# Optimization experiments

Hardware: AMD Instinct MI355X
Metric: run time of the kernel (lower is better)

Reference implementation:

```python
import jax, jax.numpy as jnp
import numpy as np

H = 256  # hidden size

def setup_inputs() -> dict:
    key = jax.random.key(0)
    k1, k2, k3 = jax.random.split(key, 3)
    B, T, D = 64, 2048, 256
    x = jax.random.normal(k1, (B, T, D), dtype=jnp.float32)
    Wx = jax.random.normal(k2, (D, 4 * H), dtype=jnp.float32) * (1.0 / np.sqrt(D))
    Wh = jax.random.normal(k3, (H, 4 * H), dtype=jnp.float32) * (1.0 / np.sqrt(H))
    bx = jnp.zeros((4 * H,), dtype=jnp.float32)
    bh = jnp.zeros((4 * H,), dtype=jnp.float32)
    return {"x": x, "Wx": Wx, "Wh": Wh, "bx": bx, "bh": bh}

def reference(x, Wx, Wh, bx, bh):
    B, T, D = x.shape
    # Precompute input projections for all timesteps: [T, B, 4H]
    xg = jnp.einsum('btd,dg->tbg', x, Wx) + bx

    def step(carry, xg_t):
        h_prev, c_prev = carry
        gates = xg_t + h_prev @ Wh + bh          # [B, 4H]
        f, i, o, chat = jnp.split(gates, 4, axis=-1)
        f_t = jax.nn.sigmoid(f)
        i_t = jax.nn.sigmoid(i)
        o_t = jax.nn.sigmoid(o)
        c_t = f_t * c_prev + i_t * jnp.tanh(chat)
        h_t = o_t * jnp.tanh(c_t)
        return (h_t, c_t), h_t

    h0 = jnp.zeros((B, H), dtype=x.dtype)
    c0 = jnp.zeros((B, H), dtype=x.dtype)
    (h_T, c_T), hs = jax.lax.scan(step, (h0, c0), xg)  # hs: [T, B, H]
    outputs = jnp.transpose(hs, (1, 0, 2))  # batch_first: [B, T, H]
    return outputs, (h_T, c_T)
```

## Files before the change

kernel.cpp:

```cpp
#include <hip/hip_runtime.h>
#include <stdint.h>

#define H 256
#define BB 64
#define TT 2048
#define G4 1024
#define LDX 264

typedef __attribute__((ext_vector_type(8))) short short8;
typedef __attribute__((ext_vector_type(4))) float float4_;
typedef unsigned long long ull;
typedef unsigned short ushort_t;
typedef unsigned int uint_t;

static __device__ __forceinline__ float bfhi2f(ushort_t u) {
    union { unsigned int i; float f; } v; v.i = ((unsigned int)u) << 16; return v.f;
}
static __device__ __forceinline__ ushort_t f2bf(float x) {
    union { float f; unsigned int i; } v; v.f = x;
    unsigned int u = v.i;
    return (ushort_t)((u + 0x7FFFu + ((u >> 16) & 1u)) >> 16);
}
static __device__ __forceinline__ void split2(float x, ushort_t& hi, ushort_t& lo) {
    hi = f2bf(x);
    lo = f2bf(x - bfhi2f(hi));
}
static __device__ __forceinline__ float sigm(float x) { return 1.0f / (1.0f + __expf(-x)); }
static __device__ __forceinline__ float tanh_(float x) { return 2.0f / (1.0f + __expf(-2.0f * x)) - 1.0f; }

__global__ __launch_bounds__(256) void split_w(const float* __restrict__ Wx,
                                               const float* __restrict__ Wh,
                                               ushort_t* __restrict__ planes) {
    const int g = blockIdx.x & 1023;
    const int mat = blockIdx.x >> 10;
    const int k = threadIdx.x;
    const float* src = mat ? Wh : Wx;
    float v = src[(size_t)k * G4 + g];
    ushort_t hi, lo; split2(v, hi, lo);
    ushort_t* ph = planes + (size_t)mat * 2 * G4 * 256;
    ph[g * 256 + k] = hi;
    ph[(size_t)G4 * 256 + g * 256 + k] = lo;
}

__global__ __launch_bounds__(256, 1) void lstm_scan(
        const float* __restrict__ x,
        const float* __restrict__ bx,
        const float* __restrict__ bh,
        const ushort_t* __restrict__ WxTh, const ushort_t* __restrict__ WxTl,
        const ushort_t* __restrict__ WhTh, const ushort_t* __restrict__ WhTl,
        float* __restrict__ out0,
        float* __restrict__ outh,
        float* __restrict__ outc,
        uint_t* __restrict__ hbuf,
        uint_t* __restrict__ ctrl) {
    __shared__ ushort_t xah[16 * LDX], xal[16 * LDX];
    __shared__ ushort_t hsh[16 * LDX], hsl[16 * LDX];
    __shared__ float gatesL[1024];
    __shared__ float cst[256];
    __shared__ float bL[64];

    const int tid = threadIdx.x;

    if (blockIdx.x >= 64) {
        float a0 = 1.0f + tid * 1e-7f, a1 = 1.1f, a2 = 1.2f, a3 = 1.3f;
        const float b = 1.0000001f, c = 1e-9f;
        for (int it = 0; it < 40000; ++it) {
#pragma unroll 32
            for (int k = 0; k < 256; ++k) {
                a0 = __builtin_fmaf(a0, b, c);
                a1 = __builtin_fmaf(a1, b, c);
                a2 = __builtin_fmaf(a2, b, c);
                a3 = __builtin_fmaf(a3, b, c);
            }
            if (__hip_atomic_load(&ctrl[0], __ATOMIC_RELAXED, __HIP_MEMORY_SCOPE_AGENT) >= 64u)
                break;
        }
        asm volatile("" :: "v"(a0), "v"(a1), "v"(a2), "v"(a3));
        return;
    }

    const int grp = blockIdx.x & 3;
    const int s = blockIdx.x >> 2;
    const int lane = tid & 63, wave = tid >> 6;
    const int lm = lane & 15, lq = lane >> 4;
    const int pb = tid >> 4, pj = tid & 15;

    if (tid < 64) {
        int g = ((tid >> 4) << 8) + (s << 4) + (tid & 15);
        bL[tid] = bx[g] + bh[g];
    }
    cst[tid] = 0.0f;

    const size_t wrow = ((size_t)((wave << 8) + (s << 4) + lm)) * 256;
    short8 fxh[8], fxl[8], fhh[8], fhl[8];
#pragma unroll
    for (int kc = 0; kc < 8; ++kc) {
        fxh[kc] = *(const short8*)(WxTh + wrow + kc * 32 + lq * 8);
        fxl[kc] = *(const short8*)(WxTl + wrow + kc * 32 + lq * 8);
        fhh[kc] = *(const short8*)(WhTh + wrow + kc * 32 + lq * 8);
        fhl[kc] = *(const short8*)(WhTl + wrow + kc * 32 + lq * 8);
    }

    const float* xp0 = x + ((size_t)(grp * 16 + pb)) * TT * 256 + pj * 16;
    float* o0 = out0 + ((size_t)(grp * 16 + pb)) * TT * H + (s << 4) + pj;

    float4_ xv[4];
#pragma unroll
    for (int q = 0; q < 4; ++q) xv[q] = *(const float4_*)(xp0 + q * 4);

    const int rb = pb * LDX + pj * 16;

    for (int t = 0; t < TT; ++t) {
#pragma unroll
        for (int q = 0; q < 4; ++q) {
            union { ushort_t u[4]; ull q8; } ph_, pl_;
#pragma unroll
            for (int e = 0; e < 4; ++e) {
                ushort_t hi, lo; split2(xv[q][e], hi, lo);
                ph_.u[e] = hi; pl_.u[e] = lo;
            }
            *(ull*)(xah + rb + q * 4) = ph_.q8;
            *(ull*)(xal + rb + q * 4) = pl_.q8;
        }
        __syncthreads();

        const uint_t* hp = hbuf + ((((t & 1) << 2) + grp) << 12) + (pb << 8) + (pj << 4);
        uint_t w[16];
        if (t > 0) {
#pragma unroll
            for (int e = 0; e < 16; ++e)
                w[e] = __hip_atomic_load(hp + e, __ATOMIC_RELAXED, __HIP_MEMORY_SCOPE_AGENT);
        }

        float4_ acc = {};
#pragma unroll
        for (int kc = 0; kc < 8; ++kc) {
            short8 ah = *(const short8*)(xah + lm * LDX + kc * 32 + lq * 8);
            short8 al = *(const short8*)(xal + lm * LDX + kc * 32 + lq * 8);
            acc = __builtin_amdgcn_mfma_f32_16x16x32_bf16(ah, fxh[kc], acc, 0, 0, 0);
            acc = __builtin_amdgcn_mfma_f32_16x16x32_bf16(ah, fxl[kc], acc, 0, 0, 0);
            acc = __builtin_amdgcn_mfma_f32_16x16x32_bf16(al, fxh[kc], acc, 0, 0, 0);
        }

        if (t > 0) {
            const uint_t texp = (uint_t)(t & 127);
            while (true) {
                bool ok = true;
#pragma unroll
                for (int e = 0; e < 16; ++e) ok &= ((w[e] & 127u) == texp);
                if (ok) break;
#pragma unroll
                for (int e = 0; e < 16; ++e)
                    w[e] = __hip_atomic_load(hp + e, __ATOMIC_RELAXED, __HIP_MEMORY_SCOPE_AGENT);
            }
        }

        if (t + 1 < TT) {
            const float* xp = xp0 + (size_t)(t + 1) * 256;
#pragma unroll
            for (int q = 0; q < 4; ++q) xv[q] = *(const float4_*)(xp + q * 4);
        }

        if (t > 0) {
#pragma unroll
            for (int q = 0; q < 4; ++q) {
                union { ushort_t u[4]; ull q8; } ph_, pl_;
#pragma unroll
                for (int e = 0; e < 4; ++e) {
                    float v = __uint_as_float(w[q * 4 + e] & ~127u);
                    ushort_t hi, lo; split2(v, hi, lo);
                    ph_.u[e] = hi; pl_.u[e] = lo;
                }
                *(ull*)(hsh + rb + q * 4) = ph_.q8;
                *(ull*)(hsl + rb + q * 4) = pl_.q8;
            }
            __syncthreads();

#pragma unroll
            for (int kc = 0; kc < 8; ++kc) {
                short8 ah = *(const short8*)(hsh + lm * LDX + kc * 32 + lq * 8);
                short8 al = *(const short8*)(hsl + lm * LDX + kc * 32 + lq * 8);
                acc = __builtin_amdgcn_mfma_f32_16x16x32_bf16(ah, fhh[kc], acc, 0, 0, 0);
                acc = __builtin_amdgcn_mfma_f32_16x16x32_bf16(ah, fhl[kc], acc, 0, 0, 0);
                acc = __builtin_amdgcn_mfma_f32_16x16x32_bf16(al, fhh[kc], acc, 0, 0, 0);
            }
        }

#pragma unroll
        for (int r = 0; r < 4; ++r)
            gatesL[(wave << 8) + ((lq * 4 + r) << 4) + lm] = acc[r];
        __syncthreads();

        float g0 = gatesL[tid]       + bL[pj];
        float g1 = gatesL[256 + tid] + bL[16 + pj];
        float g2 = gatesL[512 + tid] + bL[32 + pj];
        float g3 = gatesL[768 + tid] + bL[48 + pj];
        float ft = sigm(g0), it = sigm(g1), ot = sigm(g2), ch = tanh_(g3);
        float c = ft * cst[tid] + it * ch;
        cst[tid] = c;
        float hv = ot * tanh_(c);

        uint_t um = __float_as_uint(hv) & ~127u;
        float hm = __uint_as_float(um);
        o0[(size_t)t * H] = hm;

        uint_t* hw = hbuf + (((((t & 1) ^ 1) << 2) + grp) << 12) + (pb << 8) + (s << 4) + pj;
        __hip_atomic_store(hw, um | (uint_t)((t + 1) & 127), __ATOMIC_RELAXED, __HIP_MEMORY_SCOPE_AGENT);

        if (t == TT - 1) {
            outh[(grp * 16 + pb) * H + (s << 4) + pj] = hm;
            outc[(grp * 16 + pb) * H + (s << 4) + pj] = c;
        }
    }

    if (tid == 0)
        __hip_atomic_fetch_add(&ctrl[0], 1u, __ATOMIC_RELEASE, __HIP_MEMORY_SCOPE_AGENT);
}

extern "C" void kernel_launch(void* const* d_in, const int* in_sizes, int n_in,
                              void* d_out, int out_size, void* d_ws, size_t ws_size,
                              hipStream_t stream) {
    (void)in_sizes; (void)n_in; (void)out_size; (void)ws_size;
    const float* x  = (const float*)d_in[0];
    const float* Wx = (const float*)d_in[1];
    const float* Wh = (const float*)d_in[2];
    const float* bx = (const float*)d_in[3];
    const float* bh = (const float*)d_in[4];
    float* out0 = (float*)d_out;
    float* outh = out0 + (size_t)BB * TT * H;
    float* outc = outh + (size_t)BB * H;

    uint_t* hbuf = (uint_t*)d_ws;
    uint_t* ctrl = (uint_t*)((char*)d_ws + 131072);
    ushort_t* planes = (ushort_t*)((char*)d_ws + 131072 + 128);

    hipMemsetAsync(d_ws, 0, 131072 + 128, stream);
    split_w<<<2048, 256, 0, stream>>>(Wx, Wh, planes);
    lstm_scan<<<256, 256, 0, stream>>>(x, bx, bh,
        planes,
        planes + (size_t)G4 * 256,
        planes + (size_t)2 * G4 * 256,
        planes + (size_t)3 * G4 * 256,
        out0, outh, outc, hbuf, ctrl);
}
```

Baseline: 7.888 ms.

## Remap worker blocks across XCDs and use cache-local fast polling with fallback buffer

Launches 512 blocks and picks workers so that all 64 workers for the four batch groups land on a chosen subset of dies (b&7<4). Each h value is written twice: to a workgroup-scope buffer polled with sc0 vector loads, which are meant to hit the shared L2, and to an agent-scope mirror buffer. Polling switches to the mirror buffer for the rest of the run if the fast path times out. The aim is lower cross-block handoff latency per timestep, at the cost of relying on a block-to-XCD placement assumption, doubled stores, and more spinning filler blocks.

```diff
diff --git a/kernel.cpp b/kernel.cpp
--- a/kernel.cpp
+++ b/kernel.cpp
@@ -12,6 +12,7 @@
 typedef unsigned long long ull;
 typedef unsigned short ushort_t;
 typedef unsigned int uint_t;
+typedef __attribute__((ext_vector_type(4))) uint_t uint4_;
 
 static __device__ __forceinline__ float bfhi2f(ushort_t u) {
     union { unsigned int i; float f; } v; v.i = ((unsigned int)u) << 16; return v.f;
@@ -52,6 +53,7 @@
         float* __restrict__ outh,
         float* __restrict__ outc,
         uint_t* __restrict__ hbuf,
+        uint_t* __restrict__ mbuf,
         uint_t* __restrict__ ctrl) {
     __shared__ ushort_t xah[16 * LDX], xal[16 * LDX];
     __shared__ ushort_t hsh[16 * LDX], hsl[16 * LDX];
@@ -60,27 +62,35 @@
     __shared__ float bL[64];
 
     const int tid = threadIdx.x;
-
-    if (blockIdx.x >= 64) {
+    const int b = blockIdx.x;
+    const int isWorker = ((b & 7) < 4) && ((b >> 3) < 16);
+
+    if (!isWorker) {
+        __shared__ int bdone;
+        if (tid == 0) bdone = 0;
+        __syncthreads();
         float a0 = 1.0f + tid * 1e-7f, a1 = 1.1f, a2 = 1.2f, a3 = 1.3f;
-        const float b = 1.0000001f, c = 1e-9f;
+        const float bm = 1.0000001f, cm = 1e-9f;
         for (int it = 0; it < 40000; ++it) {
 #pragma unroll 32
             for (int k = 0; k < 256; ++k) {
-                a0 = __builtin_fmaf(a0, b, c);
-                a1 = __builtin_fmaf(a1, b, c);
-                a2 = __builtin_fmaf(a2, b, c);
-                a3 = __builtin_fmaf(a3, b, c);
-            }
-            if (__hip_atomic_load(&ctrl[0], __ATOMIC_RELAXED, __HIP_MEMORY_SCOPE_AGENT) >= 64u)
-                break;
+                a0 = __builtin_fmaf(a0, bm, cm);
+                a1 = __builtin_fmaf(a1, bm, cm);
+                a2 = __builtin_fmaf(a2, bm, cm);
+                a3 = __builtin_fmaf(a3, bm, cm);
+            }
+            if (tid == 0 &&
+                __hip_atomic_load(&ctrl[0], __ATOMIC_RELAXED, __HIP_MEMORY_SCOPE_AGENT) >= 64u)
+                bdone = 1;
+            __syncthreads();
+            if (bdone) break;
         }
         asm volatile("" :: "v"(a0), "v"(a1), "v"(a2), "v"(a3));
         return;
     }
 
-    const int grp = blockIdx.x & 3;
-    const int s = blockIdx.x >> 2;
+    const int grp = b & 7;
+    const int s = b >> 3;
     const int lane = tid & 63, wave = tid >> 6;
     const int lm = lane & 15, lq = lane >> 4;
     const int pb = tid >> 4, pj = tid & 15;
@@ -109,6 +119,7 @@
     for (int q = 0; q < 4; ++q) xv[q] = *(const float4_*)(xp0 + q * 4);
 
     const int rb = pb * LDX + pj * 16;
+    int fastpoll = 1;
 
     for (int t = 0; t < TT; ++t) {
 #pragma unroll
@@ -123,14 +134,6 @@
             *(ull*)(xal + rb + q * 4) = pl_.q8;
         }
         __syncthreads();
-
-        const uint_t* hp = hbuf + ((((t & 1) << 2) + grp) << 12) + (pb << 8) + (pj << 4);
-        uint_t w[16];
-        if (t > 0) {
-#pragma unroll
-            for (int e = 0; e < 16; ++e)
-                w[e] = __hip_atomic_load(hp + e, __ATOMIC_RELAXED, __HIP_MEMORY_SCOPE_AGENT);
-        }
 
         float4_ acc = {};
 #pragma unroll
@@ -142,16 +145,53 @@
             acc = __builtin_amdgcn_mfma_f32_16x16x32_bf16(al, fxh[kc], acc, 0, 0, 0);
         }
 
+        uint_t w[16];
         if (t > 0) {
+            const size_t ridx = ((size_t)((((t & 1) << 2) + grp) << 12)) + (pb << 8) + (pj << 4);
+            const uint_t* hp = hbuf + ridx;
+            const uint_t* mp = mbuf + ridx;
             const uint_t texp = (uint_t)(t & 127);
-            while (true) {
-                bool ok = true;
-#pragma unroll
-                for (int e = 0; e < 16; ++e) ok &= ((w[e] & 127u) == texp);
-                if (ok) break;
-#pragma unroll
-                for (int e = 0; e < 16; ++e)
-                    w[e] = __hip_atomic_load(hp + e, __ATOMIC_RELAXED, __HIP_MEMORY_SCOPE_AGENT);
+            int got = 0;
+            if (fastpoll) {
+                const int limit = (t == 1) ? 16384 : 512;
+                int rounds = 0;
+                while (rounds < limit) {
+                    uint4_ a0, a1, a2, a3;
+                    asm volatile(
+                        "global_load_dwordx4 %0, %4, off sc0\n\t"
+                        "global_load_dwordx4 %1, %4, off offset:16 sc0\n\t"
+                        "global_load_dwordx4 %2, %4, off offset:32 sc0\n\t"
+                        "global_load_dwordx4 %3, %4, off offset:48 sc0\n\t"
+                        "s_waitcnt vmcnt(0)"
+                        : "=&v"(a0), "=&v"(a1), "=&v"(a2), "=&v"(a3)
+                        : "v"(hp) : "memory");
+                    bool ok = true;
+#pragma unroll
+                    for (int e = 0; e < 4; ++e) {
+                        ok &= ((a0[e] & 127u) == texp); ok &= ((a1[e] & 127u) == texp);
+                        ok &= ((a2[e] & 127u) == texp); ok &= ((a3[e] & 127u) == texp);
+                    }
+                    if (ok) {
+#pragma unroll
+                        for (int e = 0; e < 4; ++e) {
+                            w[e] = a0[e]; w[4 + e] = a1[e]; w[8 + e] = a2[e]; w[12 + e] = a3[e];
+                        }
+                        got = 1; break;
+                    }
+                    ++rounds;
+                }
+                if (!got) fastpoll = 0;
+            }
+            if (!got) {
+                while (true) {
+                    bool ok = true;
+#pragma unroll
+                    for (int e = 0; e < 16; ++e)
+                        w[e] = __hip_atomic_load(mp + e, __ATOMIC_RELAXED, __HIP_MEMORY_SCOPE_AGENT);
+#pragma unroll
+                    for (int e = 0; e < 16; ++e) ok &= ((w[e] & 127u) == texp);
+                    if (ok) break;
+                }
             }
         }
 
@@ -204,8 +244,10 @@
         float hm = __uint_as_float(um);
         o0[(size_t)t * H] = hm;
 
-        uint_t* hw = hbuf + (((((t & 1) ^ 1) << 2) + grp) << 12) + (pb << 8) + (s << 4) + pj;
-        __hip_atomic_store(hw, um | (uint_t)((t + 1) & 127), __ATOMIC_RELAXED, __HIP_MEMORY_SCOPE_AGENT);
+        const uint_t tagged = um | (uint_t)((t + 1) & 127);
+        const size_t widx = ((size_t)(((((t & 1) ^ 1) << 2) + grp) << 12)) + (pb << 8) + (s << 4) + pj;
+        __hip_atomic_store(hbuf + widx, tagged, __ATOMIC_RELAXED, __HIP_MEMORY_SCOPE_WORKGROUP);
+        __hip_atomic_store(mbuf + widx, tagged, __ATOMIC_RELAXED, __HIP_MEMORY_SCOPE_AGENT);
 
         if (t == TT - 1) {
             outh[(grp * 16 + pb) * H + (s << 4) + pj] = hm;
@@ -231,15 +273,16 @@
     float* outc = outh + (size_t)BB * H;
 
     uint_t* hbuf = (uint_t*)d_ws;
-    uint_t* ctrl = (uint_t*)((char*)d_ws + 131072);
-    ushort_t* planes = (ushort_t*)((char*)d_ws + 131072 + 128);
-
-    hipMemsetAsync(d_ws, 0, 131072 + 128, stream);
+    uint_t* mbuf = (uint_t*)((char*)d_ws + 131072);
+    uint_t* ctrl = (uint_t*)((char*)d_ws + 262144);
+    ushort_t* planes = (ushort_t*)((char*)d_ws + 262144 + 128);
+
+    hipMemsetAsync(d_ws, 0, 262144 + 128, stream);
     split_w<<<2048, 256, 0, stream>>>(Wx, Wh, planes);
-    lstm_scan<<<256, 256, 0, stream>>>(x, bx, bh,
+    lstm_scan<<<512, 256, 0, stream>>>(x, bx, bh,
         planes,
         planes + (size_t)G4 * 256,
         planes + (size_t)2 * G4 * 256,
         planes + (size_t)3 * G4 * 256,
-        out0, outh, outc, hbuf, ctrl);
-}
+        out0, outh, outc, hbuf, mbuf, ctrl);
+}
```

After: 10.75 ms. 1.36x slower.

## Vectorize h-state polling loads, publish h before output store, rework filler blocks

Applied to the files above, without the earlier changes.

The spin-wait that polls neighbouring blocks' tagged h values now issues four 16-byte global loads with cache-bypass bits in inline asm, replacing sixteen scalar atomic loads. Each step's h value is published to the exchange buffer before the regular output store, so the consumers waiting on it can proceed sooner. The filler blocks that keep the clocks high now run eight independent FMA chains and check the completion counter less often, with one thread reading it and sharing the result through shared memory and barriers. The inline asm relies on vectorized loads of tagged words staying coherent. It also adds barriers inside the filler loop.

```diff
diff --git a/kernel.cpp b/kernel.cpp
--- a/kernel.cpp
+++ b/kernel.cpp
@@ -12,6 +12,7 @@
 typedef unsigned long long ull;
 typedef unsigned short ushort_t;
 typedef unsigned int uint_t;
+typedef __attribute__((ext_vector_type(4))) uint_t uint4_;
 
 static __device__ __forceinline__ float bfhi2f(ushort_t u) {
     union { unsigned int i; float f; } v; v.i = ((unsigned int)u) << 16; return v.f;
@@ -62,20 +63,35 @@
     const int tid = threadIdx.x;
 
     if (blockIdx.x >= 64) {
+        __shared__ int bdone;
+        if (tid == 0) bdone = 0;
+        __syncthreads();
         float a0 = 1.0f + tid * 1e-7f, a1 = 1.1f, a2 = 1.2f, a3 = 1.3f;
-        const float b = 1.0000001f, c = 1e-9f;
-        for (int it = 0; it < 40000; ++it) {
-#pragma unroll 32
-            for (int k = 0; k < 256; ++k) {
-                a0 = __builtin_fmaf(a0, b, c);
-                a1 = __builtin_fmaf(a1, b, c);
-                a2 = __builtin_fmaf(a2, b, c);
-                a3 = __builtin_fmaf(a3, b, c);
-            }
-            if (__hip_atomic_load(&ctrl[0], __ATOMIC_RELAXED, __HIP_MEMORY_SCOPE_AGENT) >= 64u)
-                break;
-        }
-        asm volatile("" :: "v"(a0), "v"(a1), "v"(a2), "v"(a3));
+        float a4 = 1.4f, a5 = 1.5f, a6 = 1.6f, a7 = 1.7f;
+        const float bm = 1.0000001f, cm = 1e-9f;
+        for (int outer = 0; outer < 20000; ++outer) {
+#pragma unroll
+            for (int k = 0; k < 128; ++k) {
+                a0 = __builtin_fmaf(a0, bm, cm);
+                a1 = __builtin_fmaf(a1, bm, cm);
+                a2 = __builtin_fmaf(a2, bm, cm);
+                a3 = __builtin_fmaf(a3, bm, cm);
+                a4 = __builtin_fmaf(a4, bm, cm);
+                a5 = __builtin_fmaf(a5, bm, cm);
+                a6 = __builtin_fmaf(a6, bm, cm);
+                a7 = __builtin_fmaf(a7, bm, cm);
+            }
+            if ((outer & 7) == 7) {
+                if (tid == 0 &&
+                    __hip_atomic_load(&ctrl[0], __ATOMIC_RELAXED, __HIP_MEMORY_SCOPE_AGENT) >= 64u)
+                    bdone = 1;
+                __syncthreads();
+                if (bdone) break;
+                __syncthreads();
+            }
+        }
+        asm volatile("" :: "v"(a0), "v"(a1), "v"(a2), "v"(a3),
+                           "v"(a4), "v"(a5), "v"(a6), "v"(a7));
         return;
     }
 
@@ -149,9 +165,19 @@
 #pragma unroll
                 for (int e = 0; e < 16; ++e) ok &= ((w[e] & 127u) == texp);
                 if (ok) break;
-#pragma unroll
-                for (int e = 0; e < 16; ++e)
-                    w[e] = __hip_atomic_load(hp + e, __ATOMIC_RELAXED, __HIP_MEMORY_SCOPE_AGENT);
+                uint4_ b0, b1, b2, b3;
+                asm volatile(
+                    "global_load_dwordx4 %0, %4, off sc0 sc1\n\t"
+                    "global_load_dwordx4 %1, %4, off offset:16 sc0 sc1\n\t"
+                    "global_load_dwordx4 %2, %4, off offset:32 sc0 sc1\n\t"
+                    "global_load_dwordx4 %3, %4, off offset:48 sc0 sc1\n\t"
+                    "s_waitcnt vmcnt(0)"
+                    : "=&v"(b0), "=&v"(b1), "=&v"(b2), "=&v"(b3)
+                    : "v"(hp) : "memory");
+#pragma unroll
+                for (int e = 0; e < 4; ++e) {
+                    w[e] = b0[e]; w[4 + e] = b1[e]; w[8 + e] = b2[e]; w[12 + e] = b3[e];
+                }
             }
         }
 
@@ -201,12 +227,12 @@
         float hv = ot * tanh_(c);
 
         uint_t um = __float_as_uint(hv) & ~127u;
+
+        uint_t* hw = hbuf + (((((t & 1) ^ 1) << 2) + grp) << 12) + (pb << 8) + (s << 4) + pj;
+        __hip_atomic_store(hw, um | (uint_t)((t + 1) & 127), __ATOMIC_RELAXED, __HIP_MEMORY_SCOPE_AGENT);
+
         float hm = __uint_as_float(um);
         o0[(size_t)t * H] = hm;
-
-        uint_t* hw = hbuf + (((((t & 1) ^ 1) << 2) + grp) << 12) + (pb << 8) + (s << 4) + pj;
-        __hip_atomic_store(hw, um | (uint_t)((t + 1) & 127), __ATOMIC_RELAXED, __HIP_MEMORY_SCOPE_AGENT);
-
         if (t == TT - 1) {
             outh[(grp * 16 + pb) * H + (s << 4) + pj] = hm;
             outc[(grp * 16 + pb) * H + (s << 4) + pj] = c;
```

After: 7.927 ms. No clear change (+0.5%).
